# Kernel tuning notes

Measured on AMD Instinct MI355X. Metric: run time of the kernel, lower is better.

## Reference

```python
import jax, jax.numpy as jnp
import numpy as np

XN = 144
YN = 144
BN_EPS = 1e-5


def setup_inputs() -> dict:
    key = jax.random.key(0)
    k1, k2, k3, k4, k5 = jax.random.split(key, 5)
    B, P, M, F, C = 8, 12000, 32, 9, 64
    pillars = jax.random.normal(k1, (B, P, M, F), dtype=jnp.float32)
    pillar_indices = jax.random.randint(k2, (B, P, 3), 0, 144, dtype=jnp.int64)
    conv_w = jax.random.normal(k3, (C, F), dtype=jnp.float32) * 0.1  # 1x1 conv, no bias
    bn_gamma = jnp.ones((C,), dtype=jnp.float32)
    bn_beta = jnp.zeros((C,), dtype=jnp.float32)
    bn_mean = jax.random.normal(k4, (C,), dtype=jnp.float32) * 0.01
    bn_var = jax.random.uniform(k5, (C,), dtype=jnp.float32, minval=0.5, maxval=1.5)
    return {"pillars": pillars, "pillar_indices": pillar_indices, "conv_w": conv_w,
            "bn_gamma": bn_gamma, "bn_beta": bn_beta, "bn_mean": bn_mean, "bn_var": bn_var}


def reference(pillars, pillar_indices, conv_w, bn_gamma, bn_beta, bn_mean, bn_var):
    # pillars: [B, P, M, F] -> 1x1 conv over feature dim -> [B, C, P, M]
    x = jnp.einsum('bpmf,cf->bcpm', pillars, conv_w)
    # BatchNorm2d (inference) + ReLU
    inv_std = jax.lax.rsqrt(bn_var + BN_EPS)
    x = (x - bn_mean[None, :, None, None]) * (bn_gamma * inv_std)[None, :, None, None] \
        + bn_beta[None, :, None, None]
    x = jax.nn.relu(x)
    # MaxPool2d((1, M)): max over points-per-pillar axis -> [B, C, P]
    feat = jnp.max(x, axis=-1)
    # Scatter pillar features into BEV canvas [C, Xn*Yn]
    y_idx = pillar_indices[:, :, 1]                      # [B, P]
    x_idx = jnp.clip(pillar_indices[:, :, 2], 0, 143)    # [B, P]
    flat_idx = y_idx * XN + x_idx                        # [B, P]

    C = feat.shape[1]

    def scatter_one(f, idx):  # f: [C, P], idx: [P]
        canvas = jnp.zeros((C, XN * YN), dtype=f.dtype)
        return canvas.at[:, idx].set(f)

    out = jax.vmap(scatter_one)(feat, flat_idx)          # [B, C, Xn*Yn]
    return out.reshape(feat.shape[0], C, XN, YN)
```

## Files before the change

### kernel.cpp

```cpp
#include <hip/hip_runtime.h>
#include <stdint.h>

#define NB 8
#define NP 12000
#define NM 32
#define NF 9
#define NC 64
#define NX 144
#define NCELL (144*144)
#define NCG 8
#define CH (NC/NCG)
#define WSTRIDE 12

#define WS_WF_OFF     0
#define WS_SHIFT_OFF  3072
#define WS_WIN_OFF    4096
#define WS_FEAT_OFF   668672
#define WS_NEED       (WS_FEAT_OFF + (size_t)NB*NP*NC*4)

__global__ void prep_kernel(const float* __restrict__ conv_w,
                            const float* __restrict__ gamma,
                            const float* __restrict__ beta,
                            const float* __restrict__ mean,
                            const float* __restrict__ var,
                            float* __restrict__ wf, float* __restrict__ shift) {
    int c = threadIdx.x;
    if (c >= NC) return;
    float sc = gamma[c] * rsqrtf(var[c] + 1e-5f);
    shift[c] = beta[c] - mean[c] * sc;
    #pragma unroll
    for (int f = 0; f < NF; ++f) wf[c * WSTRIDE + f] = conv_w[c * NF + f] * sc;
    #pragma unroll
    for (int f = NF; f < WSTRIDE; ++f) wf[c * WSTRIDE + f] = 0.f;
}

__global__ void winner_kernel(const int* __restrict__ idx, int* __restrict__ winner) {
    int t = blockIdx.x * blockDim.x + threadIdx.x;
    if (t >= NB * NP) return;
    int b = t / NP;
    int p = t - b * NP;
    int y = idx[t * 3 + 1];
    int x = idx[t * 3 + 2];
    x = x < 0 ? 0 : (x > 143 ? 143 : x);
    y = y < 0 ? 0 : (y > 143 ? 143 : y);
    atomicMax(&winner[b * NCELL + y * NX + x], p);
}

template <bool COMPACT>
__global__ void __launch_bounds__(256, 3) feat_kernel(
    const float* __restrict__ pillars,
    const int*   __restrict__ idx,
    const float* __restrict__ wf,
    const float* __restrict__ shift,
    const int*   __restrict__ winner,
    float* __restrict__ feat_ws,
    float* __restrict__ out)
{
    int t = blockIdx.x * blockDim.x + threadIdx.x;
    if (t >= NB * NP * NCG) return;
    int cg  = t & (NCG - 1);
    int pil = t >> 3;
    int b   = pil / NP;
    int p   = pil - b * NP;

    int y = idx[pil * 3 + 1];
    int x = idx[pil * 3 + 2];
    x = x < 0 ? 0 : (x > 143 ? 143 : x);
    y = y < 0 ? 0 : (y > 143 ? 143 : y);
    int cell = y * NX + x;
    if (winner[b * NCELL + cell] != p) return;

    float w[CH][NF];
    float sh[CH];
    {
        const float4* wf4 = (const float4*)wf;
        #pragma unroll
        for (int j = 0; j < CH; ++j) {
            int c = cg * CH + j;
            float4 a = wf4[c * 3 + 0], bq = wf4[c * 3 + 1], cq = wf4[c * 3 + 2];
            w[j][0]=a.x; w[j][1]=a.y; w[j][2]=a.z; w[j][3]=a.w;
            w[j][4]=bq.x; w[j][5]=bq.y; w[j][6]=bq.z; w[j][7]=bq.w;
            w[j][8]=cq.x;
            sh[j] = shift[c];
        }
    }

    float mx[CH];
    #pragma unroll
    for (int j = 0; j < CH; ++j) mx[j] = -1e30f;

    const float4* p4 = (const float4*)(pillars + (long long)pil * (NM * NF));
    #pragma unroll 2
    for (int s = 0; s < NM / 4; ++s) {
        float buf[36];
        #pragma unroll
        for (int k = 0; k < 9; ++k) {
            float4 v = p4[s * 9 + k];
            buf[k*4+0]=v.x; buf[k*4+1]=v.y; buf[k*4+2]=v.z; buf[k*4+3]=v.w;
        }
        #pragma unroll
        for (int mm = 0; mm < 4; ++mm) {
            #pragma unroll
            for (int j = 0; j < CH; ++j) {
                float acc = buf[mm*NF] * w[j][0];
                #pragma unroll
                for (int f = 1; f < NF; ++f) acc = fmaf(buf[mm*NF+f], w[j][f], acc);
                mx[j] = fmaxf(mx[j], acc);
            }
        }
    }

    float v[CH];
    #pragma unroll
    for (int j = 0; j < CH; ++j) {
        float r = mx[j] + sh[j];
        v[j] = r > 0.f ? r : 0.f;
    }

    if (COMPACT) {
        float4* dst = (float4*)(feat_ws + (long long)pil * NC + cg * CH);
        dst[0] = make_float4(v[0], v[1], v[2], v[3]);
        dst[1] = make_float4(v[4], v[5], v[6], v[7]);
    } else {
        #pragma unroll
        for (int j = 0; j < CH; ++j)
            out[((long long)(b * NC + cg * CH + j)) * NCELL + cell] = v[j];
    }
}

__global__ void scatter_kernel(const int* __restrict__ winner,
                               const float* __restrict__ feat_ws,
                               float* __restrict__ out)
{
    int t = blockIdx.x * blockDim.x + threadIdx.x;
    if (t >= NB * (NCELL / 4)) return;
    int b  = t / (NCELL / 4);
    int c4 = t - b * (NCELL / 4);
    int cellbase = c4 * 4;

    int4 wv = *(const int4*)(winner + b * NCELL + cellbase);
    long long base0 = wv.x < 0 ? -1 : ((long long)(b * NP + wv.x)) * NC;
    long long base1 = wv.y < 0 ? -1 : ((long long)(b * NP + wv.y)) * NC;
    long long base2 = wv.z < 0 ? -1 : ((long long)(b * NP + wv.z)) * NC;
    long long base3 = wv.w < 0 ? -1 : ((long long)(b * NP + wv.w)) * NC;

    const float4 z = make_float4(0.f, 0.f, 0.f, 0.f);
    #pragma unroll 4
    for (int c0 = 0; c0 < NC; c0 += 4) {
        float4 f0 = base0 < 0 ? z : *(const float4*)(feat_ws + base0 + c0);
        float4 f1 = base1 < 0 ? z : *(const float4*)(feat_ws + base1 + c0);
        float4 f2 = base2 < 0 ? z : *(const float4*)(feat_ws + base2 + c0);
        float4 f3 = base3 < 0 ? z : *(const float4*)(feat_ws + base3 + c0);
        float* o = out + ((long long)(b * NC + c0)) * NCELL + cellbase;
        *(float4*)(o + 0LL*NCELL) = make_float4(f0.x, f1.x, f2.x, f3.x);
        *(float4*)(o + 1LL*NCELL) = make_float4(f0.y, f1.y, f2.y, f3.y);
        *(float4*)(o + 2LL*NCELL) = make_float4(f0.z, f1.z, f2.z, f3.z);
        *(float4*)(o + 3LL*NCELL) = make_float4(f0.w, f1.w, f2.w, f3.w);
    }
}

extern "C" void kernel_launch(void* const* d_in, const int* in_sizes, int n_in,
                              void* d_out, int out_size, void* d_ws, size_t ws_size,
                              hipStream_t stream) {
    const float* pillars = (const float*)d_in[0];
    const int*   idx     = (const int*)d_in[1];
    const float* conv_w  = (const float*)d_in[2];
    const float* gamma   = (const float*)d_in[3];
    const float* beta    = (const float*)d_in[4];
    const float* mean    = (const float*)d_in[5];
    const float* var     = (const float*)d_in[6];
    float* out = (float*)d_out;

    char* ws = (char*)d_ws;
    float* wf      = (float*)(ws + WS_WF_OFF);
    float* shift   = (float*)(ws + WS_SHIFT_OFF);
    int*   winner  = (int*)  (ws + WS_WIN_OFF);
    float* feat_ws = (float*)(ws + WS_FEAT_OFF);

    const bool compact = ws_size >= WS_NEED;

    hipMemsetAsync(winner, 0xFF, (size_t)NB * NCELL * sizeof(int), stream);
    prep_kernel<<<1, 64, 0, stream>>>(conv_w, gamma, beta, mean, var, wf, shift);
    winner_kernel<<<(NB * NP + 255) / 256, 256, 0, stream>>>(idx, winner);

    int fthreads = NB * NP * NCG;
    if (compact) {
        feat_kernel<true><<<(fthreads + 255) / 256, 256, 0, stream>>>(
            pillars, idx, wf, shift, winner, feat_ws, out);
        int sthreads = NB * (NCELL / 4);
        scatter_kernel<<<(sthreads + 255) / 256, 256, 0, stream>>>(winner, feat_ws, out);
    } else {
        hipMemsetAsync(out, 0, (size_t)out_size * sizeof(float), stream);
        feat_kernel<false><<<(fthreads + 255) / 256, 256, 0, stream>>>(
            pillars, idx, wf, shift, winner, feat_ws, out);
    }
}
```

Before: 246.5 us.

## Compute pillar conv with bf16 MFMA and fuse prep into winner kernel

Replaces the scalar FMA feature kernel with a block-per-16-pillar kernel. Each block stages pillars into LDS as bf16 padded to K=16, then computes the 1x1 conv with 32x32x16 bf16 MFMA against a prebuilt bf16 weight fragment table, doing the max over points through accumulator reduction plus a lane shuffle. The weight and BN prep is folded into the winner kernel to drop a launch. The aim is to cut ALU time and uncoalesced per-thread pillar loads, at the cost of bf16 rounding error and of loading data for pillars that do not win their cell.

```diff
diff --git a/kernel.cpp b/kernel.cpp
--- a/kernel.cpp
+++ b/kernel.cpp
@@ -1,4 +1,5 @@
 #include <hip/hip_runtime.h>
+#include <hip/hip_bf16.h>
 #include <stdint.h>
 
 #define NB 8
@@ -8,123 +9,141 @@
 #define NC 64
 #define NX 144
 #define NCELL (144*144)
-#define NCG 8
-#define CH (NC/NCG)
-#define WSTRIDE 12
-
-#define WS_WF_OFF     0
-#define WS_SHIFT_OFF  3072
-#define WS_WIN_OFF    4096
-#define WS_FEAT_OFF   668672
-#define WS_NEED       (WS_FEAT_OFF + (size_t)NB*NP*NC*4)
-
-__global__ void prep_kernel(const float* __restrict__ conv_w,
-                            const float* __restrict__ gamma,
-                            const float* __restrict__ beta,
-                            const float* __restrict__ mean,
-                            const float* __restrict__ var,
-                            float* __restrict__ wf, float* __restrict__ shift) {
-    int c = threadIdx.x;
-    if (c >= NC) return;
-    float sc = gamma[c] * rsqrtf(var[c] + 1e-5f);
-    shift[c] = beta[c] - mean[c] * sc;
-    #pragma unroll
-    for (int f = 0; f < NF; ++f) wf[c * WSTRIDE + f] = conv_w[c * NF + f] * sc;
-    #pragma unroll
-    for (int f = NF; f < WSTRIDE; ++f) wf[c * WSTRIDE + f] = 0.f;
-}
-
-__global__ void winner_kernel(const int* __restrict__ idx, int* __restrict__ winner) {
+
+#define PCHUNK 16
+#define NCHUNK ((NB*NP)/PCHUNK)
+
+typedef __attribute__((ext_vector_type(8)))  short bfrag8;
+typedef __attribute__((ext_vector_type(16))) float accf16;
+
+#define WS_BTAB  0
+#define WS_SHIFT 2048
+#define WS_WIN   4096
+#define WS_FEAT  668672
+#define WS_NEED  (WS_FEAT + (size_t)NB*NP*NC*4)
+
+__global__ void winner_prep_kernel(const int* __restrict__ idx, int* __restrict__ winner,
+                                   const float* __restrict__ conv_w,
+                                   const float* __restrict__ gamma,
+                                   const float* __restrict__ beta,
+                                   const float* __restrict__ mean,
+                                   const float* __restrict__ var,
+                                   unsigned short* __restrict__ btab,
+                                   float* __restrict__ shift)
+{
     int t = blockIdx.x * blockDim.x + threadIdx.x;
-    if (t >= NB * NP) return;
-    int b = t / NP;
-    int p = t - b * NP;
-    int y = idx[t * 3 + 1];
-    int x = idx[t * 3 + 2];
-    x = x < 0 ? 0 : (x > 143 ? 143 : x);
-    y = y < 0 ? 0 : (y > 143 ? 143 : y);
-    atomicMax(&winner[b * NCELL + y * NX + x], p);
+    if (t < NB * NP) {
+        int b = t / NP;
+        int p = t - b * NP;
+        int y = idx[t * 3 + 1];
+        int x = idx[t * 3 + 2];
+        x = x < 0 ? 0 : (x > 143 ? 143 : x);
+        y = y < 0 ? 0 : (y > 143 ? 143 : y);
+        atomicMax(&winner[b * NCELL + y * NX + x], p);
+    }
+    if (blockIdx.x == 0) {
+        int tt = threadIdx.x;
+        if (tt < 128) {
+            int ct = tt >> 6, L = tt & 63;
+            int c  = ct * 32 + (L & 31);
+            int kq = L >> 5;
+            float sc = gamma[c] * rsqrtf(var[c] + 1e-5f);
+            unsigned short* dst = btab + (ct * 64 + L) * 8;
+            #pragma unroll
+            for (int j = 0; j < 8; ++j) {
+                int k = kq * 8 + j;
+                float w = (k < NF) ? conv_w[c * NF + k] * sc : 0.f;
+                __hip_bfloat16 h = __float2bfloat16(w);
+                dst[j] = *(unsigned short*)&h;
+            }
+        }
+        if (tt < NC) {
+            float sc = gamma[tt] * rsqrtf(var[tt] + 1e-5f);
+            shift[tt] = beta[tt] - mean[tt] * sc;
+        }
+    }
 }
 
 template <bool COMPACT>
-__global__ void __launch_bounds__(256, 3) feat_kernel(
+__global__ void __launch_bounds__(256) feat_mfma_kernel(
     const float* __restrict__ pillars,
     const int*   __restrict__ idx,
-    const float* __restrict__ wf,
+    const unsigned short* __restrict__ btab,
     const float* __restrict__ shift,
     const int*   __restrict__ winner,
     float* __restrict__ feat_ws,
     float* __restrict__ out)
 {
-    int t = blockIdx.x * blockDim.x + threadIdx.x;
-    if (t >= NB * NP * NCG) return;
-    int cg  = t & (NCG - 1);
-    int pil = t >> 3;
-    int b   = pil / NP;
-    int p   = pil - b * NP;
-
-    int y = idx[pil * 3 + 1];
-    int x = idx[pil * 3 + 2];
-    x = x < 0 ? 0 : (x > 143 ? 143 : x);
-    y = y < 0 ? 0 : (y > 143 ? 143 : y);
-    int cell = y * NX + x;
-    if (winner[b * NCELL + cell] != p) return;
-
-    float w[CH][NF];
-    float sh[CH];
-    {
-        const float4* wf4 = (const float4*)wf;
+    __shared__ unsigned short tile[PCHUNK * NM * 16];
+    int tid  = threadIdx.x;
+    int lane = tid & 63;
+    int wave = tid >> 6;
+    int chunk = blockIdx.x;
+
+    #pragma unroll
+    for (int rr = 0; rr < 2; ++rr) {
+        int r = tid + rr * 256;
+        tile[r * 16 + 9] = 0;
+        *(unsigned int*)&tile[r * 16 + 10] = 0;
+        *(unsigned int*)&tile[r * 16 + 12] = 0;
+        *(unsigned int*)&tile[r * 16 + 14] = 0;
+    }
+    const float2* src = (const float2*)(pillars + (long long)chunk * (PCHUNK * NM * NF));
+    #pragma unroll
+    for (int i = 0; i < 9; ++i) {
+        int le2 = tid + i * 256;
+        float2 v = src[le2];
+        int le = le2 * 2;
+        int r = le / 9;
+        int f = le - r * 9;
+        __hip_bfloat16 hx = __float2bfloat16(v.x);
+        tile[r * 16 + f] = *(unsigned short*)&hx;
+        int f2 = f + 1, r2 = r;
+        if (f2 == 9) { f2 = 0; r2 = r + 1; }
+        __hip_bfloat16 hy = __float2bfloat16(v.y);
+        tile[r2 * 16 + f2] = *(unsigned short*)&hy;
+    }
+    __syncthreads();
+
+    bfrag8 b0 = *(const bfrag8*)(btab + lane * 8);
+    bfrag8 b1 = *(const bfrag8*)(btab + (64 + lane) * 8);
+    float  sh = shift[lane];
+
+    int row = lane & 31;
+    int kq  = lane >> 5;
+
+    #pragma unroll
+    for (int i = 0; i < 4; ++i) {
+        int pr  = wave * 4 + i;
+        int pil = chunk * PCHUNK + pr;
+        int b   = pil / NP;
+        int p   = pil - b * NP;
+        int y = idx[pil * 3 + 1];
+        int x = idx[pil * 3 + 2];
+        x = x < 0 ? 0 : (x > 143 ? 143 : x);
+        y = y < 0 ? 0 : (y > 143 ? 143 : y);
+        int cell = y * NX + x;
+        if (winner[b * NCELL + cell] != p) continue;
+
+        bfrag8 a = *(const bfrag8*)&tile[pr * 512 + row * 16 + kq * 8];
+        accf16 z = (accf16)0.0f;
+        accf16 acc0 = __builtin_amdgcn_mfma_f32_32x32x16_bf16(a, b0, z, 0, 0, 0);
+        accf16 acc1 = __builtin_amdgcn_mfma_f32_32x32x16_bf16(a, b1, z, 0, 0, 0);
+
+        float v0 = acc0[0], v1 = acc1[0];
         #pragma unroll
-        for (int j = 0; j < CH; ++j) {
-            int c = cg * CH + j;
-            float4 a = wf4[c * 3 + 0], bq = wf4[c * 3 + 1], cq = wf4[c * 3 + 2];
-            w[j][0]=a.x; w[j][1]=a.y; w[j][2]=a.z; w[j][3]=a.w;
-            w[j][4]=bq.x; w[j][5]=bq.y; w[j][6]=bq.z; w[j][7]=bq.w;
-            w[j][8]=cq.x;
-            sh[j] = shift[c];
+        for (int j = 1; j < 16; ++j) { v0 = fmaxf(v0, acc0[j]); v1 = fmaxf(v1, acc1[j]); }
+        v0 = fmaxf(v0, __shfl_xor(v0, 32));
+        v1 = fmaxf(v1, __shfl_xor(v1, 32));
+        float r = (lane < 32) ? v0 : v1;
+        r = r + sh;
+        r = r > 0.f ? r : 0.f;
+
+        if (COMPACT) {
+            feat_ws[(long long)pil * NC + lane] = r;
+        } else {
+            out[((long long)(b * NC + lane)) * NCELL + cell] = r;
         }
-    }
-
-    float mx[CH];
-    #pragma unroll
-    for (int j = 0; j < CH; ++j) mx[j] = -1e30f;
-
-    const float4* p4 = (const float4*)(pillars + (long long)pil * (NM * NF));
-    #pragma unroll 2
-    for (int s = 0; s < NM / 4; ++s) {
-        float buf[36];
-        #pragma unroll
-        for (int k = 0; k < 9; ++k) {
-            float4 v = p4[s * 9 + k];
-            buf[k*4+0]=v.x; buf[k*4+1]=v.y; buf[k*4+2]=v.z; buf[k*4+3]=v.w;
-        }
-        #pragma unroll
-        for (int mm = 0; mm < 4; ++mm) {
-            #pragma unroll
-            for (int j = 0; j < CH; ++j) {
-                float acc = buf[mm*NF] * w[j][0];
-                #pragma unroll
-                for (int f = 1; f < NF; ++f) acc = fmaf(buf[mm*NF+f], w[j][f], acc);
-                mx[j] = fmaxf(mx[j], acc);
-            }
-        }
-    }
-
-    float v[CH];
-    #pragma unroll
-    for (int j = 0; j < CH; ++j) {
-        float r = mx[j] + sh[j];
-        v[j] = r > 0.f ? r : 0.f;
-    }
-
-    if (COMPACT) {
-        float4* dst = (float4*)(feat_ws + (long long)pil * NC + cg * CH);
-        dst[0] = make_float4(v[0], v[1], v[2], v[3]);
-        dst[1] = make_float4(v[4], v[5], v[6], v[7]);
-    } else {
-        #pragma unroll
-        for (int j = 0; j < CH; ++j)
-            out[((long long)(b * NC + cg * CH + j)) * NCELL + cell] = v[j];
     }
 }
 
@@ -152,10 +171,10 @@
         float4 f2 = base2 < 0 ? z : *(const float4*)(feat_ws + base2 + c0);
         float4 f3 = base3 < 0 ? z : *(const float4*)(feat_ws + base3 + c0);
         float* o = out + ((long long)(b * NC + c0)) * NCELL + cellbase;
-        *(float4*)(o + 0LL*NCELL) = make_float4(f0.x, f1.x, f2.x, f3.x);
-        *(float4*)(o + 1LL*NCELL) = make_float4(f0.y, f1.y, f2.y, f3.y);
-        *(float4*)(o + 2LL*NCELL) = make_float4(f0.z, f1.z, f2.z, f3.z);
-        *(float4*)(o + 3LL*NCELL) = make_float4(f0.w, f1.w, f2.w, f3.w);
+        *(float4*)(o + 0LL * NCELL) = make_float4(f0.x, f1.x, f2.x, f3.x);
+        *(float4*)(o + 1LL * NCELL) = make_float4(f0.y, f1.y, f2.y, f3.y);
+        *(float4*)(o + 2LL * NCELL) = make_float4(f0.z, f1.z, f2.z, f3.z);
+        *(float4*)(o + 3LL * NCELL) = make_float4(f0.w, f1.w, f2.w, f3.w);
     }
 }
 
@@ -172,26 +191,25 @@
     float* out = (float*)d_out;
 
     char* ws = (char*)d_ws;
-    float* wf      = (float*)(ws + WS_WF_OFF);
-    float* shift   = (float*)(ws + WS_SHIFT_OFF);
-    int*   winner  = (int*)  (ws + WS_WIN_OFF);
-    float* feat_ws = (float*)(ws + WS_FEAT_OFF);
+    unsigned short* btab  = (unsigned short*)(ws + WS_BTAB);
+    float*          shift = (float*)(ws + WS_SHIFT);
+    int*            winner = (int*)(ws + WS_WIN);
+    float*          feat_ws = (float*)(ws + WS_FEAT);
 
     const bool compact = ws_size >= WS_NEED;
 
     hipMemsetAsync(winner, 0xFF, (size_t)NB * NCELL * sizeof(int), stream);
-    prep_kernel<<<1, 64, 0, stream>>>(conv_w, gamma, beta, mean, var, wf, shift);
-    winner_kernel<<<(NB * NP + 255) / 256, 256, 0, stream>>>(idx, winner);
-
-    int fthreads = NB * NP * NCG;
+    winner_prep_kernel<<<(NB * NP + 255) / 256, 256, 0, stream>>>(
+        idx, winner, conv_w, gamma, beta, mean, var, btab, shift);
+
     if (compact) {
-        feat_kernel<true><<<(fthreads + 255) / 256, 256, 0, stream>>>(
-            pillars, idx, wf, shift, winner, feat_ws, out);
-        int sthreads = NB * (NCELL / 4);
-        scatter_kernel<<<(sthreads + 255) / 256, 256, 0, stream>>>(winner, feat_ws, out);
+        feat_mfma_kernel<true><<<NCHUNK, 256, 0, stream>>>(
+            pillars, idx, btab, shift, winner, feat_ws, out);
+        scatter_kernel<<<(NB * (NCELL / 4) + 255) / 256, 256, 0, stream>>>(
+            winner, feat_ws, out);
     } else {
         hipMemsetAsync(out, 0, (size_t)out_size * sizeof(float), stream);
-        feat_kernel<false><<<(fthreads + 255) / 256, 256, 0, stream>>>(
-            pillars, idx, wf, shift, winner, feat_ws, out);
-    }
-}
+        feat_mfma_kernel<false><<<NCHUNK, 256, 0, stream>>>(
+            pillars, idx, btab, shift, winner, feat_ws, out);
+    }
+}
```

New measurement: 211.0 us. -14.4%, faster.
